# Optimization experiments

Hardware: AMD Instinct MI355X
Metric: run time of the kernel (lower is better)

The kernel has to match this reference:

```python
import jax, jax.numpy as jnp
import numpy as np

N_DYADIC = 0   # init kwarg n: dyadic refinement order (0 = no refinement)


def _sig_kernel_gram(X, Y):
    """Signature-kernel Gram matrix via Goursat PDE solve (solver=0, linear kernel).

    X: (A, M, D), Y: (B, N, D). Returns K: (A, B) with K[a,b] = k_sig(x^a, y^b).
    PDE scheme: K[i+1,j+1] = K[i+1,j] + K[i,j+1] + K[i,j]*(inc[i,j] - 1),
    K[0,:] = K[:,0] = 1, inc[i,j] = <x_{i+1}-x_i, y_{j+1}-y_j>.
    The j-recursion is a prefix sum, so each row update is a vectorized cumsum;
    only the i-direction is sequential (lax.scan over M-1 rows).
    """
    dtype = X.dtype
    dX = X[:, 1:, :] - X[:, :-1, :]          # (A, M-1, D)
    dY = Y[:, 1:, :] - Y[:, :-1, :]          # (B, N-1, D)
    inc = jnp.einsum('amd,bnd->abmn', dX, dY)  # (A, B, M-1, N-1) increment grid
    if N_DYADIC > 0:
        f = 2 ** N_DYADIC
        inc = jnp.repeat(jnp.repeat(inc, f, axis=2), f, axis=3) / (f * f)
    A, B, M1, N1 = inc.shape
    ones_col = jnp.ones((A, B, 1), dtype)
    k0 = jnp.ones((A, B, N1 + 1), dtype)      # boundary row K[0, :] = 1

    def step(k_prev, inc_row):
        # k_new[j+1] = k_new[j] + (k_prev[j+1] - k_prev[j] + k_prev[j]*inc[j])
        delta = k_prev[..., 1:] - k_prev[..., :-1] + k_prev[..., :-1] * inc_row
        k_new = jnp.concatenate([ones_col, 1.0 + jnp.cumsum(delta, axis=-1)], axis=-1)
        return k_new, None

    k_last, _ = jax.lax.scan(step, k0, jnp.moveaxis(inc, 2, 0))
    return k_last[..., -1]                    # (A, B): K(s=T, t=T)


def setup_inputs() -> dict:
    key = jax.random.key(0)
    kx, ky = jax.random.split(key)
    # scale 0.1 keeps path increments moderate so the PDE solution stays well-conditioned
    X = jax.random.normal(kx, (64, 128, 64), dtype=jnp.float32) * 0.1
    Y = jax.random.normal(ky, (64, 128, 64), dtype=jnp.float32) * 0.1
    return {"X": X, "Y": Y}


def reference(X, Y):
    K_XX = _sig_kernel_gram(X, X)
    K_YY = _sig_kernel_gram(Y, Y)
    K_XY = _sig_kernel_gram(X, Y)
    dist = jnp.mean(K_XX) + jnp.mean(K_YY) - 2.0 * jnp.mean(K_XY)
    return jnp.mean((X[:, 0, :] - Y[:, 0, :]) ** 2) + dist
```

## Files before the change

### kernel.cpp

```cpp
#include <hip/hip_runtime.h>

#define AA   64
#define MM   128
#define DD   64
#define M1   127
#define CSTR 132
#define NXY  1024
#define NTRI 544
#define NBLK (NXY + 2*NTRI)
#define REG_I4 65536
#define PART_OFF (4u << 20)

typedef float f32x4 __attribute__((ext_vector_type(4)));
typedef short bf8_t __attribute__((ext_vector_type(8)));

template <int CTRL, int RM>
__device__ __forceinline__ float dpp0(float x) {
    return __int_as_float(
        __builtin_amdgcn_update_dpp(0, __float_as_int(x), CTRL, RM, 0xF, false));
}

__device__ __forceinline__ unsigned bf16_rne(float v) {
    unsigned u = __float_as_uint(v);
    return (u + 0x7FFFu + ((u >> 16) & 1u)) >> 16;
}
__device__ __forceinline__ float bf16_tof(unsigned h) {
    return __uint_as_float(h << 16);
}

__device__ __forceinline__ void lds_fence() {
    asm volatile("s_waitcnt lgkmcnt(0)" ::: "memory");
    __builtin_amdgcn_sched_barrier(0);
}

__global__ __launch_bounds__(256) void prep_frags(const float* __restrict__ X,
                                                  const float* __restrict__ Y,
                                                  int4* __restrict__ frag) {
    const int tid = threadIdx.x, lane = tid & 63, w = tid >> 6;
    const int W    = blockIdx.x * 4 + w;
    const int inp  = W >> 9;
    const int p    = (W >> 3) & 63;
    const int tile = W & 7;
    const float* S = (inp ? Y : X) + p * (MM * DD);
    int i = tile * 16 + (lane & 15);
    if (i > 126) i = 126;
    const int d0 = (lane >> 4) << 3;

    int4* hi = frag + (inp * 2 + 0) * REG_I4;
    int4* lo = frag + (inp * 2 + 1) * REG_I4;
    const int base = p * 1024 + tile * 128 + lane;

    #pragma unroll
    for (int ks = 0; ks < 2; ++ks) {
        const float* r0 = S + i * DD + ks * 32 + d0;
        const float* r1 = r0 + DD;
        float4 a0 = *(const float4*)r0;
        float4 a1 = *(const float4*)(r0 + 4);
        float4 c0 = *(const float4*)r1;
        float4 c1 = *(const float4*)(r1 + 4);
        float v[8] = {c0.x - a0.x, c0.y - a0.y, c0.z - a0.z, c0.w - a0.w,
                      c1.x - a1.x, c1.y - a1.y, c1.z - a1.z, c1.w - a1.w};
        unsigned hs[8], ls[8];
        #pragma unroll
        for (int e = 0; e < 8; ++e) {
            hs[e] = bf16_rne(v[e]);
            ls[e] = bf16_rne(v[e] - bf16_tof(hs[e]));
        }
        int4 h, l;
        h.x = hs[0] | (hs[1] << 16); h.y = hs[2] | (hs[3] << 16);
        h.z = hs[4] | (hs[5] << 16); h.w = hs[6] | (hs[7] << 16);
        l.x = ls[0] | (ls[1] << 16); l.y = ls[2] | (ls[3] << 16);
        l.z = ls[4] | (ls[5] << 16); l.w = ls[6] | (ls[7] << 16);
        hi[base + ks * 64] = h;
        lo[base + ks * 64] = l;
    }
}

template <int ROWS>
__device__ __forceinline__ void load_sv(const float* incW, int c2l, float2* sv) {
    #pragma unroll
    for (int r = 0; r < ROWS; ++r)
        sv[r] = *(const float2*)(incW + r * CSTR + c2l);
}

template <int ROWS>
__device__ __forceinline__ void chain_sv(const float2* sv, int lane,
                                         float& Sv, float& e0p, float& e1p) {
    #pragma unroll
    for (int r = 0; r < ROWS; ++r) {
        float s0 = sv[r].x;
        float s1 = (lane < 63) ? sv[r].y : 0.0f;
        float Sp  = dpp0<0x138, 0xF>(Sv);
        float k0v = 1.0f + Sp;
        float k1v = 1.0f + Sv - e1p;
        float e0  = fmaf(k0v, s0, e0p);
        float e1  = fmaf(k1v, s1, e1p);
        float S   = e0 + e1;
        S += dpp0<0x111, 0xF>(S);
        S += dpp0<0x112, 0xF>(S);
        S += dpp0<0x114, 0xF>(S);
        S += dpp0<0x118, 0xF>(S);
        S += dpp0<0x142, 0xA>(S);
        S += dpp0<0x143, 0xC>(S);
        Sv = S; e0p = e0; e1p = e1;
    }
}

__global__ __launch_bounds__(256, 3)
void sig_pde(const int4* __restrict__ frag, float* __restrict__ partials) {
    const int tid = threadIdx.x, lane = tid & 63, w = tid >> 6;
    const int gid = blockIdx.x;

    int a, b, ain, bin;
    float wgt;
    if (gid < NXY) {
        b = gid >> 4; a = ((gid & 15) << 2) | w;
        ain = 0; bin = 1;
        wgt = -2.0f / 4096.0f;
    } else {
        int t = gid - NXY;
        int inp = 0;
        if (t >= NTRI) { t -= NTRI; inp = 1; }
        int q = (int)((__builtin_sqrtf((float)(2 * t + 1)) - 1.0f) * 0.5f);
        while (2 * (q + 1) * (q + 2) <= t) ++q;
        while (q > 0 && 2 * q * (q + 1) > t) --q;
        int r  = t - 2 * q * (q + 1);
        int i  = r / (q + 1);
        int ag = r - i * (q + 1);
        b = 4 * q + i; a = 4 * ag + w;
        ain = bin = inp;
        wgt = (a < b) ? (2.0f / 4096.0f) : ((a == b) ? (1.0f / 4096.0f) : 0.0f);
    }

    __shared__ int4  Bh[1024], Bl[1024];
    __shared__ float incS[4][8 * CSTR];
    __shared__ float red4[4];

    {
        const int4* Bhg = frag + (bin * 2 + 0) * REG_I4 + b * 1024;
        const int4* Blg = frag + (bin * 2 + 1) * REG_I4 + b * 1024;
        #pragma unroll
        for (int c = 0; c < 4; ++c) {
            int idx = c * 256 + tid;
            Bh[idx] = Bhg[idx];
            Bl[idx] = Blg[idx];
        }
    }
    __syncthreads();

    const int4* Ahg = frag + (ain * 2 + 0) * REG_I4 + a * 1024;
    const int4* Alg = frag + (ain * 2 + 1) * REG_I4 + a * 1024;

    int4 Ah[2], Al[2], Ahn[2], Aln[2];
    f32x4 acc[8];
    float Sv = 0.0f, e0p = 0.0f, e1p = 0.0f;

    float* incW = &incS[w][0];
    const int c2l = lane << 1;
    const int r0w = (lane >> 4) << 2, c0w = lane & 15;

#define MFMA_STRIP() do {                                                       \
    _Pragma("unroll")                                                           \
    for (int t_ = 0; t_ < 8; ++t_) acc[t_] = (f32x4){0.f, 0.f, 0.f, 0.f};       \
    _Pragma("unroll")                                                           \
    for (int s_ = 0; s_ < 2; ++s_) {                                            \
        bf8_t ah = __builtin_bit_cast(bf8_t, Ah[s_]);                           \
        bf8_t al = __builtin_bit_cast(bf8_t, Al[s_]);                           \
        _Pragma("unroll")                                                       \
        for (int t_ = 0; t_ < 8; ++t_) {                                        \
            int fb = (t_ * 2 + s_) * 64 + lane;                                 \
            bf8_t bh = *(const bf8_t*)&Bh[fb];                                  \
            bf8_t bl = *(const bf8_t*)&Bl[fb];                                  \
            acc[t_] = __builtin_amdgcn_mfma_f32_16x16x32_bf16(ah, bh, acc[t_], 0, 0, 0); \
            acc[t_] = __builtin_amdgcn_mfma_f32_16x16x32_bf16(ah, bl, acc[t_], 0, 0, 0); \
            acc[t_] = __builtin_amdgcn_mfma_f32_16x16x32_bf16(al, bh, acc[t_], 0, 0, 0); \
        }                                                                       \
    }                                                                           \
} while (0)

#define STORE_H(half) do {                                     \
    if ((r0w & 8) == ((half) << 3)) {                          \
        float* pb = incW + (r0w & 7) * CSTR + c0w;             \
        _Pragma("unroll")                                      \
        for (int t_ = 0; t_ < 8; ++t_) {                       \
            float* q = pb + (t_ << 4);                         \
            q[0]        = acc[t_][0];                          \
            q[CSTR]     = acc[t_][1];                          \
            q[2 * CSTR] = acc[t_][2];                          \
            q[3 * CSTR] = acc[t_][3];                          \
        }                                                      \
    }                                                          \
} while (0)

#define LOAD_A_N(poff) do {                                    \
    int off = (poff) + lane;                                   \
    Ahn[0] = Ahg[off]; Ahn[1] = Ahg[off + 64];                 \
    Aln[0] = Alg[off]; Aln[1] = Alg[off + 64];                 \
} while (0)

    Ah[0] = Ahg[lane]; Ah[1] = Ahg[64 + lane];
    Al[0] = Alg[lane]; Al[1] = Alg[64 + lane];
    MFMA_STRIP();

    for (int s = 0; s < 8; ++s) {
        if (s < 7) LOAD_A_N((s + 1) * 128);

        float2 svA[8];
        lds_fence(); STORE_H(0);
        load_sv<8>(incW, c2l, svA);
        lds_fence(); STORE_H(1);

        if (s < 7) {
            float2 svB[8];
            load_sv<8>(incW, c2l, svB);
            chain_sv<8>(svA, lane, Sv, e0p, e1p);
            Ah[0] = Ahn[0]; Ah[1] = Ahn[1];
            Al[0] = Aln[0]; Al[1] = Aln[1];
            MFMA_STRIP();
            chain_sv<8>(svB, lane, Sv, e0p, e1p);
        } else {
            float2 svB[7];
            load_sv<7>(incW, c2l, svB);
            chain_sv<8>(svA, lane, Sv, e0p, e1p);
            chain_sv<7>(svB, lane, Sv, e0p, e1p);
        }
    }

    if (lane == 63) red4[w] = wgt * (1.0f + Sv - e1p);
    __syncthreads();
    if (tid == 0)
        partials[gid] = red4[0] + red4[1] + red4[2] + red4[3];

#undef MFMA_STRIP
#undef STORE_H
#undef LOAD_A_N
}

__global__ void final_sum(const float* __restrict__ X, const float* __restrict__ Y,
                          const float* __restrict__ partials, float* __restrict__ out) {
    __shared__ float red[4];
    int tid = threadIdx.x;
    float acc = 0.f;
    for (int e = tid; e < NBLK; e += 256) acc += partials[e];
    for (int e = tid; e < AA * DD; e += 256) {
        int aa = e >> 6, d = e & 63;
        float df = X[aa * (MM * DD) + d] - Y[aa * (MM * DD) + d];
        acc = fmaf(df * df, 1.0f / 4096.0f, acc);
    }
    #pragma unroll
    for (int off = 32; off > 0; off >>= 1) acc += __shfl_down(acc, off);
    if ((tid & 63) == 0) red[tid >> 6] = acc;
    __syncthreads();
    if (tid == 0) out[0] = red[0] + red[1] + red[2] + red[3];
}

extern "C" void kernel_launch(void* const* d_in, const int* in_sizes, int n_in,
                              void* d_out, int out_size, void* d_ws, size_t ws_size,
                              hipStream_t stream) {
    const float* X = (const float*)d_in[0];
    const float* Y = (const float*)d_in[1];
    float* out = (float*)d_out;
    int4*  frag = (int4*)d_ws;
    float* partials = (float*)((char*)d_ws + PART_OFF);

    hipLaunchKernelGGL(prep_frags, dim3(256), dim3(256), 0, stream, X, Y, frag);
    hipLaunchKernelGGL(sig_pde, dim3(NBLK), dim3(256), 0, stream, frag, partials);
    hipLaunchKernelGGL(final_sum, dim3(1), dim3(256), 0, stream, X, Y, partials, out);
}
```

Before: 142.9 us.

## Process two signature-kernel pairs per wave with interleaved scan chains

```diff
diff --git a/kernel.cpp b/kernel.cpp
--- a/kernel.cpp
+++ b/kernel.cpp
@@ -3,10 +3,9 @@
 #define AA   64
 #define MM   128
 #define DD   64
-#define M1   127
 #define CSTR 132
-#define NXY  1024
-#define NTRI 544
+#define NXY  512
+#define NTRI 288
 #define NBLK (NXY + 2*NTRI)
 #define REG_I4 65536
 #define PART_OFF (4u << 20)
@@ -77,64 +76,74 @@
 }
 
 template <int ROWS>
-__device__ __forceinline__ void load_sv(const float* incW, int c2l, float2* sv) {
+__device__ __forceinline__ void load_sv(const float* buf, int c2l, float2* sv) {
     #pragma unroll
     for (int r = 0; r < ROWS; ++r)
-        sv[r] = *(const float2*)(incW + r * CSTR + c2l);
+        sv[r] = *(const float2*)(buf + r * CSTR + c2l);
 }
 
 template <int ROWS>
-__device__ __forceinline__ void chain_sv(const float2* sv, int lane,
-                                         float& Sv, float& e0p, float& e1p) {
+__device__ __forceinline__ void chain2_sv(const float2* svP, const float2* svQ,
+                                          int lane,
+                                          float& S0, float& e00, float& e10,
+                                          float& S1, float& e01, float& e11) {
     #pragma unroll
     for (int r = 0; r < ROWS; ++r) {
-        float s0 = sv[r].x;
-        float s1 = (lane < 63) ? sv[r].y : 0.0f;
-        float Sp  = dpp0<0x138, 0xF>(Sv);
-        float k0v = 1.0f + Sp;
-        float k1v = 1.0f + Sv - e1p;
-        float e0  = fmaf(k0v, s0, e0p);
-        float e1  = fmaf(k1v, s1, e1p);
-        float S   = e0 + e1;
-        S += dpp0<0x111, 0xF>(S);
-        S += dpp0<0x112, 0xF>(S);
-        S += dpp0<0x114, 0xF>(S);
-        S += dpp0<0x118, 0xF>(S);
-        S += dpp0<0x142, 0xA>(S);
-        S += dpp0<0x143, 0xC>(S);
-        Sv = S; e0p = e0; e1p = e1;
-    }
-}
-
-__global__ __launch_bounds__(256, 3)
+        float s0a = svP[r].x, s1a = (lane < 63) ? svP[r].y : 0.0f;
+        float s0b = svQ[r].x, s1b = (lane < 63) ? svQ[r].y : 0.0f;
+        float Spa = dpp0<0x138, 0xF>(S0);
+        float Spb = dpp0<0x138, 0xF>(S1);
+        float k0a = 1.0f + Spa, k1a = 1.0f + S0 - e10;
+        float k0b = 1.0f + Spb, k1b = 1.0f + S1 - e11;
+        float e0a = fmaf(k0a, s0a, e00), e1a = fmaf(k1a, s1a, e10);
+        float e0b = fmaf(k0b, s0b, e01), e1b = fmaf(k1b, s1b, e11);
+        float Sa = e0a + e1a;
+        float Sb = e0b + e1b;
+        Sa += dpp0<0x111, 0xF>(Sa);  Sb += dpp0<0x111, 0xF>(Sb);
+        Sa += dpp0<0x112, 0xF>(Sa);  Sb += dpp0<0x112, 0xF>(Sb);
+        Sa += dpp0<0x114, 0xF>(Sa);  Sb += dpp0<0x114, 0xF>(Sb);
+        Sa += dpp0<0x118, 0xF>(Sa);  Sb += dpp0<0x118, 0xF>(Sb);
+        Sa += dpp0<0x142, 0xA>(Sa);  Sb += dpp0<0x142, 0xA>(Sb);
+        Sa += dpp0<0x143, 0xC>(Sa);  Sb += dpp0<0x143, 0xC>(Sb);
+        S0 = Sa; e00 = e0a; e10 = e1a;
+        S1 = Sb; e01 = e0b; e11 = e1b;
+    }
+}
+
+__global__ __launch_bounds__(256, 2)
 void sig_pde(const int4* __restrict__ frag, float* __restrict__ partials) {
     const int tid = threadIdx.x, lane = tid & 63, w = tid >> 6;
     const int gid = blockIdx.x;
 
-    int a, b, ain, bin;
-    float wgt;
+    int b, a0, a1, ain, bin;
+    float wgt0, wgt1;
     if (gid < NXY) {
-        b = gid >> 4; a = ((gid & 15) << 2) | w;
+        b = gid >> 3;
+        int abase = (gid & 7) * 8;
+        a0 = abase + 2 * w; a1 = a0 + 1;
         ain = 0; bin = 1;
-        wgt = -2.0f / 4096.0f;
+        wgt0 = wgt1 = -2.0f / 4096.0f;
     } else {
         int t = gid - NXY;
         int inp = 0;
         if (t >= NTRI) { t -= NTRI; inp = 1; }
-        int q = (int)((__builtin_sqrtf((float)(2 * t + 1)) - 1.0f) * 0.5f);
-        while (2 * (q + 1) * (q + 2) <= t) ++q;
-        while (q > 0 && 2 * q * (q + 1) > t) --q;
-        int r  = t - 2 * q * (q + 1);
-        int i  = r / (q + 1);
-        int ag = r - i * (q + 1);
-        b = 4 * q + i; a = 4 * ag + w;
+        int g = (int)((__builtin_sqrtf((float)(t + 1)) - 1.0f) * 0.5f);
+        while (4 * (g + 1) * (g + 2) <= t) ++g;
+        while (g > 0 && 4 * g * (g + 1) > t) --g;
+        int r  = t - 4 * g * (g + 1);
+        int bi = r / (g + 1);
+        int c  = r - bi * (g + 1);
+        b = 8 * g + bi;
+        int abase = c * 8;
+        a0 = abase + 2 * w; a1 = a0 + 1;
         ain = bin = inp;
-        wgt = (a < b) ? (2.0f / 4096.0f) : ((a == b) ? (1.0f / 4096.0f) : 0.0f);
+        wgt0 = (a0 < b) ? (2.0f / 4096.0f) : ((a0 == b) ? (1.0f / 4096.0f) : 0.0f);
+        wgt1 = (a1 < b) ? (2.0f / 4096.0f) : ((a1 == b) ? (1.0f / 4096.0f) : 0.0f);
     }
 
     __shared__ int4  Bh[1024], Bl[1024];
-    __shared__ float incS[4][8 * CSTR];
-    __shared__ float red4[4];
+    __shared__ float incS[8][8 * CSTR];
+    __shared__ float red8[8];
 
     {
         const int4* Bhg = frag + (bin * 2 + 0) * REG_I4 + b * 1024;
@@ -148,90 +157,115 @@
     }
     __syncthreads();
 
-    const int4* Ahg = frag + (ain * 2 + 0) * REG_I4 + a * 1024;
-    const int4* Alg = frag + (ain * 2 + 1) * REG_I4 + a * 1024;
-
-    int4 Ah[2], Al[2], Ahn[2], Aln[2];
-    f32x4 acc[8];
-    float Sv = 0.0f, e0p = 0.0f, e1p = 0.0f;
-
-    float* incW = &incS[w][0];
+    const int4* Ahg0 = frag + (ain * 2 + 0) * REG_I4 + a0 * 1024;
+    const int4* Alg0 = frag + (ain * 2 + 1) * REG_I4 + a0 * 1024;
+    const int4* Ahg1 = frag + (ain * 2 + 0) * REG_I4 + a1 * 1024;
+    const int4* Alg1 = frag + (ain * 2 + 1) * REG_I4 + a1 * 1024;
+
+    int4 A0h[2], A0l[2], A1h[2], A1l[2];
+    int4 N0h[2], N0l[2], N1h[2], N1l[2];
+    f32x4 acc[2][8];
+    float S0 = 0.f, e00 = 0.f, e10 = 0.f;
+    float S1 = 0.f, e01 = 0.f, e11 = 0.f;
+
+    float* buf0 = &incS[2 * w + 0][0];
+    float* buf1 = &incS[2 * w + 1][0];
     const int c2l = lane << 1;
     const int r0w = (lane >> 4) << 2, c0w = lane & 15;
 
-#define MFMA_STRIP() do {                                                       \
+#define MFMA_PASS() do {                                                        \
     _Pragma("unroll")                                                           \
-    for (int t_ = 0; t_ < 8; ++t_) acc[t_] = (f32x4){0.f, 0.f, 0.f, 0.f};       \
+    for (int p_ = 0; p_ < 2; ++p_)                                              \
+        _Pragma("unroll")                                                       \
+        for (int t_ = 0; t_ < 8; ++t_) acc[p_][t_] = (f32x4){0.f,0.f,0.f,0.f};  \
     _Pragma("unroll")                                                           \
     for (int s_ = 0; s_ < 2; ++s_) {                                            \
-        bf8_t ah = __builtin_bit_cast(bf8_t, Ah[s_]);                           \
-        bf8_t al = __builtin_bit_cast(bf8_t, Al[s_]);                           \
+        bf8_t ah0 = __builtin_bit_cast(bf8_t, A0h[s_]);                         \
+        bf8_t al0 = __builtin_bit_cast(bf8_t, A0l[s_]);                         \
+        bf8_t ah1 = __builtin_bit_cast(bf8_t, A1h[s_]);                         \
+        bf8_t al1 = __builtin_bit_cast(bf8_t, A1l[s_]);                         \
         _Pragma("unroll")                                                       \
         for (int t_ = 0; t_ < 8; ++t_) {                                        \
             int fb = (t_ * 2 + s_) * 64 + lane;                                 \
             bf8_t bh = *(const bf8_t*)&Bh[fb];                                  \
             bf8_t bl = *(const bf8_t*)&Bl[fb];                                  \
-            acc[t_] = __builtin_amdgcn_mfma_f32_16x16x32_bf16(ah, bh, acc[t_], 0, 0, 0); \
-            acc[t_] = __builtin_amdgcn_mfma_f32_16x16x32_bf16(ah, bl, acc[t_], 0, 0, 0); \
-            acc[t_] = __builtin_amdgcn_mfma_f32_16x16x32_bf16(al, bh, acc[t_], 0, 0, 0); \
+            acc[0][t_] = __builtin_amdgcn_mfma_f32_16x16x32_bf16(ah0, bh, acc[0][t_], 0, 0, 0); \
+            acc[1][t_] = __builtin_amdgcn_mfma_f32_16x16x32_bf16(ah1, bh, acc[1][t_], 0, 0, 0); \
+            acc[0][t_] = __builtin_amdgcn_mfma_f32_16x16x32_bf16(ah0, bl, acc[0][t_], 0, 0, 0); \
+            acc[1][t_] = __builtin_amdgcn_mfma_f32_16x16x32_bf16(ah1, bl, acc[1][t_], 0, 0, 0); \
+            acc[0][t_] = __builtin_amdgcn_mfma_f32_16x16x32_bf16(al0, bh, acc[0][t_], 0, 0, 0); \
+            acc[1][t_] = __builtin_amdgcn_mfma_f32_16x16x32_bf16(al1, bh, acc[1][t_], 0, 0, 0); \
         }                                                                       \
     }                                                                           \
 } while (0)
 
-#define STORE_H(half) do {                                     \
+#define STORE_H(p, half, buf) do {                             \
     if ((r0w & 8) == ((half) << 3)) {                          \
-        float* pb = incW + (r0w & 7) * CSTR + c0w;             \
+        float* pb = (buf) + (r0w & 7) * CSTR + c0w;            \
         _Pragma("unroll")                                      \
         for (int t_ = 0; t_ < 8; ++t_) {                       \
             float* q = pb + (t_ << 4);                         \
-            q[0]        = acc[t_][0];                          \
-            q[CSTR]     = acc[t_][1];                          \
-            q[2 * CSTR] = acc[t_][2];                          \
-            q[3 * CSTR] = acc[t_][3];                          \
+            q[0]        = acc[p][t_][0];                       \
+            q[CSTR]     = acc[p][t_][1];                       \
+            q[2 * CSTR] = acc[p][t_][2];                       \
+            q[3 * CSTR] = acc[p][t_][3];                       \
         }                                                      \
     }                                                          \
 } while (0)
 
 #define LOAD_A_N(poff) do {                                    \
     int off = (poff) + lane;                                   \
-    Ahn[0] = Ahg[off]; Ahn[1] = Ahg[off + 64];                 \
-    Aln[0] = Alg[off]; Aln[1] = Alg[off + 64];                 \
+    N0h[0] = Ahg0[off]; N0h[1] = Ahg0[off + 64];               \
+    N0l[0] = Alg0[off]; N0l[1] = Alg0[off + 64];               \
+    N1h[0] = Ahg1[off]; N1h[1] = Ahg1[off + 64];               \
+    N1l[0] = Alg1[off]; N1l[1] = Alg1[off + 64];               \
 } while (0)
 
-    Ah[0] = Ahg[lane]; Ah[1] = Ahg[64 + lane];
-    Al[0] = Alg[lane]; Al[1] = Alg[64 + lane];
-    MFMA_STRIP();
+    A0h[0] = Ahg0[lane]; A0h[1] = Ahg0[64 + lane];
+    A0l[0] = Alg0[lane]; A0l[1] = Alg0[64 + lane];
+    A1h[0] = Ahg1[lane]; A1h[1] = Ahg1[64 + lane];
+    A1l[0] = Alg1[lane]; A1l[1] = Alg1[64 + lane];
+    MFMA_PASS();
 
     for (int s = 0; s < 8; ++s) {
         if (s < 7) LOAD_A_N((s + 1) * 128);
 
-        float2 svA[8];
-        lds_fence(); STORE_H(0);
-        load_sv<8>(incW, c2l, svA);
-        lds_fence(); STORE_H(1);
-
+        float2 sv00[8], sv10[8];
+        lds_fence();
+        STORE_H(0, 0, buf0); load_sv<8>(buf0, c2l, sv00);
+        STORE_H(1, 0, buf1); load_sv<8>(buf1, c2l, sv10);
+        chain2_sv<8>(sv00, sv10, lane, S0, e00, e10, S1, e01, e11);
+
+        lds_fence();
         if (s < 7) {
-            float2 svB[8];
-            load_sv<8>(incW, c2l, svB);
-            chain_sv<8>(svA, lane, Sv, e0p, e1p);
-            Ah[0] = Ahn[0]; Ah[1] = Ahn[1];
-            Al[0] = Aln[0]; Al[1] = Aln[1];
-            MFMA_STRIP();
-            chain_sv<8>(svB, lane, Sv, e0p, e1p);
+            float2 sv01[8], sv11[8];
+            STORE_H(0, 1, buf0); load_sv<8>(buf0, c2l, sv01);
+            STORE_H(1, 1, buf1); load_sv<8>(buf1, c2l, sv11);
+            A0h[0] = N0h[0]; A0h[1] = N0h[1]; A0l[0] = N0l[0]; A0l[1] = N0l[1];
+            A1h[0] = N1h[0]; A1h[1] = N1h[1]; A1l[0] = N1l[0]; A1l[1] = N1l[1];
+            MFMA_PASS();
+            chain2_sv<8>(sv01, sv11, lane, S0, e00, e10, S1, e01, e11);
         } else {
-            float2 svB[7];
-            load_sv<7>(incW, c2l, svB);
-            chain_sv<8>(svA, lane, Sv, e0p, e1p);
-            chain_sv<7>(svB, lane, Sv, e0p, e1p);
+            float2 sv01[7], sv11[7];
+            STORE_H(0, 1, buf0); load_sv<7>(buf0, c2l, sv01);
+            STORE_H(1, 1, buf1); load_sv<7>(buf1, c2l, sv11);
+            chain2_sv<7>(sv01, sv11, lane, S0, e00, e10, S1, e01, e11);
         }
     }
 
-    if (lane == 63) red4[w] = wgt * (1.0f + Sv - e1p);
+    if (lane == 63) {
+        red8[2 * w + 0] = wgt0 * (1.0f + S0 - e10);
+        red8[2 * w + 1] = wgt1 * (1.0f + S1 - e11);
+    }
     __syncthreads();
-    if (tid == 0)
-        partials[gid] = red4[0] + red4[1] + red4[2] + red4[3];
-
-#undef MFMA_STRIP
+    if (tid == 0) {
+        float r = 0.f;
+        #pragma unroll
+        for (int i = 0; i < 8; ++i) r += red8[i];
+        partials[gid] = r;
+    }
+
+#undef MFMA_PASS
 #undef STORE_H
 #undef LOAD_A_N
 }
```

Result: slower. 165.3 us (+15.7%).

## Fuse bf16 split-fragment preparation into the PDE kernel and drop prep launch

Applied to the files above, without the earlier changes.

```diff
diff --git a/kernel.cpp b/kernel.cpp
--- a/kernel.cpp
+++ b/kernel.cpp
@@ -3,13 +3,10 @@
 #define AA   64
 #define MM   128
 #define DD   64
-#define M1   127
 #define CSTR 132
 #define NXY  1024
 #define NTRI 544
 #define NBLK (NXY + 2*NTRI)
-#define REG_I4 65536
-#define PART_OFF (4u << 20)
 
 typedef float f32x4 __attribute__((ext_vector_type(4)));
 typedef short bf8_t __attribute__((ext_vector_type(8)));
@@ -33,47 +30,21 @@
     __builtin_amdgcn_sched_barrier(0);
 }
 
-__global__ __launch_bounds__(256) void prep_frags(const float* __restrict__ X,
-                                                  const float* __restrict__ Y,
-                                                  int4* __restrict__ frag) {
-    const int tid = threadIdx.x, lane = tid & 63, w = tid >> 6;
-    const int W    = blockIdx.x * 4 + w;
-    const int inp  = W >> 9;
-    const int p    = (W >> 3) & 63;
-    const int tile = W & 7;
-    const float* S = (inp ? Y : X) + p * (MM * DD);
-    int i = tile * 16 + (lane & 15);
-    if (i > 126) i = 126;
-    const int d0 = (lane >> 4) << 3;
-
-    int4* hi = frag + (inp * 2 + 0) * REG_I4;
-    int4* lo = frag + (inp * 2 + 1) * REG_I4;
-    const int base = p * 1024 + tile * 128 + lane;
-
-    #pragma unroll
-    for (int ks = 0; ks < 2; ++ks) {
-        const float* r0 = S + i * DD + ks * 32 + d0;
-        const float* r1 = r0 + DD;
-        float4 a0 = *(const float4*)r0;
-        float4 a1 = *(const float4*)(r0 + 4);
-        float4 c0 = *(const float4*)r1;
-        float4 c1 = *(const float4*)(r1 + 4);
-        float v[8] = {c0.x - a0.x, c0.y - a0.y, c0.z - a0.z, c0.w - a0.w,
-                      c1.x - a1.x, c1.y - a1.y, c1.z - a1.z, c1.w - a1.w};
-        unsigned hs[8], ls[8];
-        #pragma unroll
-        for (int e = 0; e < 8; ++e) {
-            hs[e] = bf16_rne(v[e]);
-            ls[e] = bf16_rne(v[e] - bf16_tof(hs[e]));
-        }
-        int4 h, l;
-        h.x = hs[0] | (hs[1] << 16); h.y = hs[2] | (hs[3] << 16);
-        h.z = hs[4] | (hs[5] << 16); h.w = hs[6] | (hs[7] << 16);
-        l.x = ls[0] | (ls[1] << 16); l.y = ls[2] | (ls[3] << 16);
-        l.z = ls[4] | (ls[5] << 16); l.w = ls[6] | (ls[7] << 16);
-        hi[base + ks * 64] = h;
-        lo[base + ks * 64] = l;
-    }
+__device__ __forceinline__ void cvt8(const float4& a0, const float4& a1,
+                                     const float4& c0, const float4& c1,
+                                     int4& h, int4& l) {
+    float v[8] = {c0.x - a0.x, c0.y - a0.y, c0.z - a0.z, c0.w - a0.w,
+                  c1.x - a1.x, c1.y - a1.y, c1.z - a1.z, c1.w - a1.w};
+    unsigned hs[8], ls[8];
+    #pragma unroll
+    for (int e = 0; e < 8; ++e) {
+        hs[e] = bf16_rne(v[e]);
+        ls[e] = bf16_rne(v[e] - bf16_tof(hs[e]));
+    }
+    h.x = hs[0] | (hs[1] << 16); h.y = hs[2] | (hs[3] << 16);
+    h.z = hs[4] | (hs[5] << 16); h.w = hs[6] | (hs[7] << 16);
+    l.x = ls[0] | (ls[1] << 16); l.y = ls[2] | (ls[3] << 16);
+    l.z = ls[4] | (ls[5] << 16); l.w = ls[6] | (ls[7] << 16);
 }
 
 template <int ROWS>
@@ -107,7 +78,8 @@
 }
 
 __global__ __launch_bounds__(256, 3)
-void sig_pde(const int4* __restrict__ frag, float* __restrict__ partials) {
+void sig_pde(const float* __restrict__ X, const float* __restrict__ Y,
+             float* __restrict__ partials) {
     const int tid = threadIdx.x, lane = tid & 63, w = tid >> 6;
     const int gid = blockIdx.x;
 
@@ -137,27 +109,59 @@
     __shared__ float red4[4];
 
     {
-        const int4* Bhg = frag + (bin * 2 + 0) * REG_I4 + b * 1024;
-        const int4* Blg = frag + (bin * 2 + 1) * REG_I4 + b * 1024;
+        const float* Sb = (bin ? Y : X) + b * (MM * DD);
         #pragma unroll
         for (int c = 0; c < 4; ++c) {
-            int idx = c * 256 + tid;
-            Bh[idx] = Bhg[idx];
-            Bl[idx] = Blg[idx];
+            int e    = c * 256 + tid;
+            int tile = e >> 7;
+            int rest = e & 127;
+            int ks   = rest >> 6;
+            int lb   = rest & 63;
+            int i    = tile * 16 + (lb & 15);
+            if (i > 126) i = 126;
+            const float* r0 = Sb + i * DD + ((lb >> 4) << 3) + ks * 32;
+            float4 a0 = *(const float4*)r0;
+            float4 a1 = *(const float4*)(r0 + 4);
+            float4 c0 = *(const float4*)(r0 + DD);
+            float4 c1 = *(const float4*)(r0 + DD + 4);
+            int4 h, l;
+            cvt8(a0, a1, c0, c1, h, l);
+            Bh[e] = h;
+            Bl[e] = l;
         }
     }
     __syncthreads();
 
-    const int4* Ahg = frag + (ain * 2 + 0) * REG_I4 + a * 1024;
-    const int4* Alg = frag + (ain * 2 + 1) * REG_I4 + a * 1024;
-
-    int4 Ah[2], Al[2], Ahn[2], Aln[2];
+    const float* Sa = (ain ? Y : X) + a * (MM * DD);
+    const int d0a = (lane >> 4) << 3;
+
+    int4 Ah[2], Al[2];
+    float4 F[8];
     f32x4 acc[8];
     float Sv = 0.0f, e0p = 0.0f, e1p = 0.0f;
 
     float* incW = &incS[w][0];
     const int c2l = lane << 1;
     const int r0w = (lane >> 4) << 2, c0w = lane & 15;
+
+#define LOADRAW(sidx) do {                                     \
+    int i_ = (sidx) * 16 + (lane & 15);                        \
+    if (i_ > 126) i_ = 126;                                    \
+    const float* p0 = Sa + i_ * DD + d0a;                      \
+    F[0] = *(const float4*)p0;                                 \
+    F[1] = *(const float4*)(p0 + 4);                           \
+    F[2] = *(const float4*)(p0 + DD);                          \
+    F[3] = *(const float4*)(p0 + DD + 4);                      \
+    F[4] = *(const float4*)(p0 + 32);                          \
+    F[5] = *(const float4*)(p0 + 36);                          \
+    F[6] = *(const float4*)(p0 + DD + 32);                     \
+    F[7] = *(const float4*)(p0 + DD + 36);                     \
+} while (0)
+
+#define CONV_A() do {                                          \
+    cvt8(F[0], F[1], F[2], F[3], Ah[0], Al[0]);                \
+    cvt8(F[4], F[5], F[6], F[7], Ah[1], Al[1]);                \
+} while (0)
 
 #define MFMA_STRIP() do {                                                       \
     _Pragma("unroll")                                                           \
@@ -192,18 +196,12 @@
     }                                                          \
 } while (0)
 
-#define LOAD_A_N(poff) do {                                    \
-    int off = (poff) + lane;                                   \
-    Ahn[0] = Ahg[off]; Ahn[1] = Ahg[off + 64];                 \
-    Aln[0] = Alg[off]; Aln[1] = Alg[off + 64];                 \
-} while (0)
-
-    Ah[0] = Ahg[lane]; Ah[1] = Ahg[64 + lane];
-    Al[0] = Alg[lane]; Al[1] = Alg[64 + lane];
+    LOADRAW(0);
+    CONV_A();
     MFMA_STRIP();
 
     for (int s = 0; s < 8; ++s) {
-        if (s < 7) LOAD_A_N((s + 1) * 128);
+        if (s < 7) LOADRAW(s + 1);
 
         float2 svA[8];
         lds_fence(); STORE_H(0);
@@ -214,8 +212,7 @@
             float2 svB[8];
             load_sv<8>(incW, c2l, svB);
             chain_sv<8>(svA, lane, Sv, e0p, e1p);
-            Ah[0] = Ahn[0]; Ah[1] = Ahn[1];
-            Al[0] = Aln[0]; Al[1] = Aln[1];
+            CONV_A();
             MFMA_STRIP();
             chain_sv<8>(svB, lane, Sv, e0p, e1p);
         } else {
@@ -231,9 +228,10 @@
     if (tid == 0)
         partials[gid] = red4[0] + red4[1] + red4[2] + red4[3];
 
+#undef LOADRAW
+#undef CONV_A
 #undef MFMA_STRIP
 #undef STORE_H
-#undef LOAD_A_N
 }
 
 __global__ void final_sum(const float* __restrict__ X, const float* __restrict__ Y,
@@ -260,10 +258,8 @@
     const float* X = (const float*)d_in[0];
     const float* Y = (const float*)d_in[1];
     float* out = (float*)d_out;
-    int4*  frag = (int4*)d_ws;
-    float* partials = (float*)((char*)d_ws + PART_OFF);
-
-    hipLaunchKernelGGL(prep_frags, dim3(256), dim3(256), 0, stream, X, Y, frag);
-    hipLaunchKernelGGL(sig_pde, dim3(NBLK), dim3(256), 0, stream, frag, partials);
+    float* partials = (float*)d_ws;
+
+    hipLaunchKernelGGL(sig_pde, dim3(NBLK), dim3(256), 0, stream, X, Y, partials);
     hipLaunchKernelGGL(final_sum, dim3(1), dim3(256), 0, stream, X, Y, partials, out);
 }
```

Measured after the change: 186.5 us. 30.5% more time.
